# Performance work log

Measured on AMD Instinct MI355X. Metric: run time of the kernel, lower is better.

Reference implementation:

```python
import jax, jax.numpy as jnp
import numpy as np

ETA = 0.01   # Hebbian learning rate of the plasticity rule
LR = 1.0     # CircuitModel.lr


def setup_inputs() -> dict:
    key = jax.random.key(0)
    k1, k2, k3 = jax.random.split(key, 3)
    B, T, NI, NO, NOBS = 64, 256, 512, 512, 128
    X = jax.random.normal(k1, (B, T, NI), dtype=jnp.float32)
    W_init = jax.random.normal(k2, (B, NO, NI), dtype=jnp.float32) * 0.1
    observed_idx = jnp.sort(jax.random.randint(k3, (NOBS,), 0, NO))
    return {"X": X, "W_init": W_init, "observed_idx": observed_idx}


def reference(X, W_init, observed_idx):
    # X: [B,T,NI], W_init: [B,NO,NI], observed_idx: [NOBS] int
    NO = W_init.shape[1]
    mask = jnp.zeros((NO,), X.dtype).at[observed_idx].set(1.0)  # [NO]

    def step(W, x_t):
        # x_t: [B,NI]
        pre = jnp.einsum('boi,bi->bo', W, x_t)          # [B,NO]
        y = jax.nn.sigmoid(pre)
        m = y[:, observed_idx]                           # [B,NOBS] recorded before masking
        y_sparse = y * mask                              # zero unobserved outputs
        W = W * mask[None, :, None]                      # zero unobserved rows of W
        dW = ETA * (y_sparse[:, :, None] * x_t[:, None, :])  # Hebbian outer product
        return W + LR * dW, m

    _, m_traj = jax.lax.scan(step, W_init, jnp.swapaxes(X, 0, 1))  # [T,B,NOBS]
    return jnp.swapaxes(m_traj, 0, 1)  # [B,T,NOBS]
```

## Files before the change

### kernel.cpp

```cpp
#include <hip/hip_runtime.h>

#define NB   64
#define NT   256
#define NI   512
#define NO   512
#define NOBS 128
#define ETA  0.01f

typedef __attribute__((ext_vector_type(8))) short bf16x8;
typedef __attribute__((ext_vector_type(4))) float f32x4;

#define X4_COUNT  (NB*NT*NI/4)
#define WG4_COUNT (NB*NOBS*NI/4)
#define K0_TOTAL  (X4_COUNT + WG4_COUNT)

__device__ __forceinline__ unsigned short f2bf(float f) {
    unsigned int u = __float_as_uint(f);
    return (unsigned short)((u + 0x7fffu + ((u >> 16) & 1u)) >> 16);
}

__global__ __launch_bounds__(256)
void k0_convert(const float* __restrict__ X, const float* __restrict__ Wi,
                const int* __restrict__ obs,
                unsigned short* __restrict__ Xb, unsigned short* __restrict__ Wg)
{
    int idx = blockIdx.x * 256 + threadIdx.x;
    const int stride = gridDim.x * 256;
    for (; idx < K0_TOTAL; idx += stride) {
        float4 v; ushort4* dst;
        if (idx < X4_COUNT) {
            v = ((const float4*)X)[idx];
            dst = (ushort4*)Xb + idx;
        } else {
            int g = idx - X4_COUNT;
            int row = g >> 7, pos = g & 127;
            int b = row >> 7, j = row & 127;
            v = ((const float4*)(Wi + ((size_t)b * NO + obs[j]) * NI))[pos];
            dst = (ushort4*)Wg + ((size_t)row * 128 + pos);
        }
        *dst = make_ushort4(f2bf(v.x), f2bf(v.y), f2bf(v.z), f2bf(v.w));
    }
}

__global__ __launch_bounds__(256)
void k1_gemm(const unsigned short* __restrict__ Xb,
             const unsigned short* __restrict__ Wg,
             float* __restrict__ Gd, unsigned short* __restrict__ Gh,
             float* __restrict__ P0)
{
    __shared__ unsigned short As[128 * 64];
    __shared__ unsigned short Bs[128 * 64];

    const int tid  = threadIdx.x;
    const int lane = tid & 63;
    const int wv   = tid >> 6;
    const int l16  = lane & 15;
    const int quad = lane >> 4;

    const int b   = blockIdx.x & 63;
    const int sub = blockIdx.x >> 6;

    const unsigned short* xbB = Xb + (size_t)b * NT * NI;
    const unsigned short *aRows, *bRows;
    int bm = 0, bn = 0;
    if (sub < 3) {
        bm = (sub >= 1) ? 1 : 0;
        bn = (sub == 2) ? 1 : 0;
        aRows = xbB + (size_t)bm * 128 * NI;
        bRows = xbB + (size_t)bn * 128 * NI;
    } else {
        const int pb = sub - 3;
        bm = pb;
        aRows = xbB + (size_t)pb * 128 * NI;
        bRows = Wg + (size_t)b * NOBS * NI;
    }

    const int wm = (wv >> 1) * 64;
    const int wn = (wv & 1) * 64;

    f32x4 acc[4][4] = {};

    for (int kb = 0; kb < NI / 64; ++kb) {
        __syncthreads();
#pragma unroll
        for (int it = 0; it < 4; ++it) {
            const int s = it * 256 + tid;
            const int m = s >> 3, c = s & 7;
            const int slot = m * 64 + ((c ^ (m & 7)) * 8);
            const size_t goff = (size_t)m * NI + kb * 64 + c * 8;
            *(bf16x8*)&As[slot] = *(const bf16x8*)(aRows + goff);
            *(bf16x8*)&Bs[slot] = *(const bf16x8*)(bRows + goff);
        }
        __syncthreads();
#pragma unroll
        for (int ks = 0; ks < 2; ++ks) {
            const int q = ks * 4 + quad;
            bf16x8 af[4], bfr[4];
#pragma unroll
            for (int mt = 0; mt < 4; ++mt) {
                const int m = wm + mt * 16 + l16;
                af[mt] = *(const bf16x8*)&As[m * 64 + ((q ^ (m & 7)) * 8)];
            }
#pragma unroll
            for (int nt = 0; nt < 4; ++nt) {
                const int n = wn + nt * 16 + l16;
                bfr[nt] = *(const bf16x8*)&Bs[n * 64 + ((q ^ (n & 7)) * 8)];
            }
#pragma unroll
            for (int mt = 0; mt < 4; ++mt)
#pragma unroll
                for (int nt = 0; nt < 4; ++nt)
                    acc[mt][nt] = __builtin_amdgcn_mfma_f32_16x16x32_bf16(
                        af[mt], bfr[nt], acc[mt][nt], 0, 0, 0);
        }
    }

    if (sub < 3) {
        unsigned short* GhB = Gh + ((size_t)b << 16);
        float* GdB = Gd + ((size_t)b << 12);
#pragma unroll
        for (int mt = 0; mt < 4; ++mt)
#pragma unroll
            for (int nt = 0; nt < 4; ++nt) {
                const int gcol = bn * 128 + wn + nt * 16 + l16;
#pragma unroll
                for (int r = 0; r < 4; ++r) {
                    const int grow = bm * 128 + wm + mt * 16 + quad * 4 + r;
                    const float v = acc[mt][nt][r];
                    GhB[(size_t)grow * 256 + gcol] = f2bf(v);
                    if ((grow >> 4) == (gcol >> 4))
                        GdB[((grow >> 4) << 8) + ((grow & 15) << 4) + (gcol & 15)] = v;
                }
            }
    } else {
        float* Pb = P0 + (size_t)b * NT * NOBS + (size_t)bm * 128 * NOBS;
#pragma unroll
        for (int mt = 0; mt < 4; ++mt)
#pragma unroll
            for (int nt = 0; nt < 4; ++nt)
#pragma unroll
                for (int r = 0; r < 4; ++r)
                    Pb[(size_t)(wm + mt * 16 + quad * 4 + r) * NOBS
                       + wn + nt * 16 + l16] = acc[mt][nt][r];
    }
}

__global__ __launch_bounds__(512)
void k2_scan(const float* __restrict__ Gd, const unsigned short* __restrict__ Gh,
             const float* __restrict__ P0, float* __restrict__ out)
{
    __shared__ float gdiag[16 * 16 * 16];
    __shared__ float preS[16 * 32];
    __shared__ unsigned int ybf2[2 * 8 * 32];

    const int tid  = threadIdx.x;
    const int lane = tid & 63;
    const int l16  = lane & 15;
    const int quad = lane >> 4;
    const int w    = __builtin_amdgcn_readfirstlane(tid >> 6);

    const int b  = blockIdx.x & 63;
    const int jg = blockIdx.x >> 6;

    const float* Pb = P0 + (size_t)b * NT * NOBS + jg * 32;
    const unsigned short* GhB = Gh + ((size_t)b << 16);
    float* ob = out + (size_t)b * NT * NOBS + jg * 32;

    {
        const f32x4* gs = (const f32x4*)(Gd + ((size_t)b << 12));
        ((f32x4*)gdiag)[tid]       = gs[tid];
        ((f32x4*)gdiag)[512 + tid] = gs[512 + tid];
    }

    f32x4 acc[2][2];
#pragma unroll
    for (int s2 = 0; s2 < 2; ++s2)
#pragma unroll
        for (int nt = 0; nt < 2; ++nt)
#pragma unroll
            for (int r = 0; r < 4; ++r)
                acc[s2][nt][r] =
                    Pb[(size_t)(w * 32 + s2 * 16 + quad * 4 + r) * NOBS
                       + nt * 16 + l16];

#pragma unroll
    for (int c = 0; c < 16; ++c) {
        const int cp = c & 1;
        if (w == (c >> 1)) {
#pragma unroll
            for (int nt = 0; nt < 2; ++nt)
#pragma unroll
                for (int r = 0; r < 4; ++r)
                    preS[(quad * 4 + r) * 32 + nt * 16 + l16] = acc[cp][nt][r];
        }
        __syncthreads();
        if (w == (c >> 1) && lane < 32) {
            const int j = lane;
            float p[16];
#pragma unroll
            for (int u = 0; u < 16; ++u) p[u] = preS[u * 32 + j];
            const float* gdc = gdiag + c * 256;
            float eprev = 0.f;
#pragma unroll
            for (int u = 0; u < 16; ++u) {
                const float y = 1.f / (1.f + __expf(-p[u]));
                ob[(size_t)(c * 16 + u) * NOBS + j] = y;
                const float e = ETA * y;
#pragma unroll
                for (int v = u + 1; v < 16; ++v)
                    p[v] = fmaf(e, gdc[u * 16 + v], p[v]);
                if (u & 1)
                    ybf2[cp * 256 + (u >> 1) * 32 + j] =
                        (unsigned)f2bf(eprev) | ((unsigned)f2bf(e) << 16);
                else
                    eprev = e;
            }
        }
        __syncthreads();
        if (c < 15) {
            union { bf16x8 v; unsigned int d[4]; } B0, B1;
#pragma unroll
            for (int p2 = 0; p2 < 4; ++p2) { B0.d[p2] = 0; B1.d[p2] = 0; }
            if (quad < 2) {
#pragma unroll
                for (int p2 = 0; p2 < 4; ++p2) {
                    B0.d[p2] = ybf2[cp * 256 + (quad * 4 + p2) * 32 + l16];
                    B1.d[p2] = ybf2[cp * 256 + (quad * 4 + p2) * 32 + 16 + l16];
                }
            }
#pragma unroll
            for (int s2 = 0; s2 < 2; ++s2) {
                const int T = 2 * w + s2;
                if (T > c) {
                    union { bf16x8 v; unsigned int d[4]; } A;
#pragma unroll
                    for (int p2 = 0; p2 < 4; ++p2) A.d[p2] = 0;
                    if (quad < 2)
                        A.v = *(const bf16x8*)(GhB + (size_t)(T * 16 + l16) * 256
                                               + c * 16 + quad * 8);
                    acc[s2][0] = __builtin_amdgcn_mfma_f32_16x16x32_bf16(
                        A.v, B0.v, acc[s2][0], 0, 0, 0);
                    acc[s2][1] = __builtin_amdgcn_mfma_f32_16x16x32_bf16(
                        A.v, B1.v, acc[s2][1], 0, 0, 0);
                }
            }
        }
    }
}

extern "C" void kernel_launch(void* const* d_in, const int* in_sizes, int n_in,
                              void* d_out, int out_size, void* d_ws, size_t ws_size,
                              hipStream_t stream)
{
    const float* X   = (const float*)d_in[0];
    const float* Wi  = (const float*)d_in[1];
    const int*   obs = (const int*)d_in[2];
    float*       out = (float*)d_out;

    float*          Gd = (float*)d_ws;
    float*          P0 = (float*)((char*)d_ws + (1u << 20));
    unsigned short* Gh = (unsigned short*)((char*)d_ws + (9u << 20));
    unsigned short* Xb = (unsigned short*)((char*)d_ws + (17u << 20));
    unsigned short* Wg = (unsigned short*)((char*)d_ws + (33u << 20));

    hipLaunchKernelGGL(k0_convert, dim3(3072), dim3(256), 0, stream,
                       X, Wi, obs, Xb, Wg);
    hipLaunchKernelGGL(k1_gemm, dim3(NB * 5), dim3(256), 0, stream,
                       Xb, Wg, Gd, Gh, P0);
    hipLaunchKernelGGL(k2_scan, dim3(NB * 4), dim3(512), 0, stream,
                       Gd, Gh, P0, out);
}
```

Baseline: 168.1 us.

## Collapse scan kernel to one wavefront with register-held bf16 Hebbian history

Rewrites k2_scan from 8 wavefronts with two block barriers per chunk to a single 64-lane wavefront. Each 16-step chunk gathers its correction from earlier chunks by MFMA over a K=32 history kept in registers (Bf). That history is refreshed every two chunks, and the odd chunk adds a half-K MFMA for its immediate predecessor. This removes __syncthreads overhead and cross-wave handoff latency on the sequential path. In exchange the block is much smaller, the GPU has far fewer active waves, and register pressure rises.

```diff
diff --git a/kernel.cpp b/kernel.cpp
--- a/kernel.cpp
+++ b/kernel.cpp
@@ -145,19 +145,17 @@
     }
 }
 
-__global__ __launch_bounds__(512)
+__global__ __launch_bounds__(64)
 void k2_scan(const float* __restrict__ Gd, const unsigned short* __restrict__ Gh,
              const float* __restrict__ P0, float* __restrict__ out)
 {
-    __shared__ float gdiag[16 * 16 * 16];
-    __shared__ float preS[16 * 32];
-    __shared__ unsigned int ybf2[2 * 8 * 32];
-
-    const int tid  = threadIdx.x;
-    const int lane = tid & 63;
+    __shared__ float gdiag[16 * 256];
+    __shared__ unsigned short ybuf[32 * 32];
+    __shared__ float preS[16 * 33];
+
+    const int lane = threadIdx.x;
     const int l16  = lane & 15;
     const int quad = lane >> 4;
-    const int w    = __builtin_amdgcn_readfirstlane(tid >> 6);
 
     const int b  = blockIdx.x & 63;
     const int jg = blockIdx.x >> 6;
@@ -168,82 +166,90 @@
 
     {
         const f32x4* gs = (const f32x4*)(Gd + ((size_t)b << 12));
-        ((f32x4*)gdiag)[tid]       = gs[tid];
-        ((f32x4*)gdiag)[512 + tid] = gs[512 + tid];
-    }
-
-    f32x4 acc[2][2];
-#pragma unroll
-    for (int s2 = 0; s2 < 2; ++s2)
+#pragma unroll
+        for (int p = 0; p < 16; ++p)
+            ((f32x4*)gdiag)[p * 64 + lane] = gs[p * 64 + lane];
+    }
+
+    bf16x8 Bf[8][2];
+
+#pragma unroll
+    for (int T = 0; T < 16; ++T) {
+        f32x4 acc[2];
 #pragma unroll
         for (int nt = 0; nt < 2; ++nt)
 #pragma unroll
             for (int r = 0; r < 4; ++r)
-                acc[s2][nt][r] =
-                    Pb[(size_t)(w * 32 + s2 * 16 + quad * 4 + r) * NOBS
-                       + nt * 16 + l16];
-
-#pragma unroll
-    for (int c = 0; c < 16; ++c) {
-        const int cp = c & 1;
-        if (w == (c >> 1)) {
-#pragma unroll
-            for (int nt = 0; nt < 2; ++nt)
-#pragma unroll
-                for (int r = 0; r < 4; ++r)
-                    preS[(quad * 4 + r) * 32 + nt * 16 + l16] = acc[cp][nt][r];
-        }
-        __syncthreads();
-        if (w == (c >> 1) && lane < 32) {
+                acc[nt][r] = Pb[(size_t)(T * 16 + quad * 4 + r) * NOBS
+                                + nt * 16 + l16];
+
+#pragma unroll
+        for (int p = 0; p < 8; ++p)
+            if (p < (T >> 1)) {
+                const bf16x8 A = *(const bf16x8*)(
+                    GhB + (size_t)(T * 16 + l16) * 256 + p * 32 + quad * 8);
+                acc[0] = __builtin_amdgcn_mfma_f32_16x16x32_bf16(
+                    A, Bf[p][0], acc[0], 0, 0, 0);
+                acc[1] = __builtin_amdgcn_mfma_f32_16x16x32_bf16(
+                    A, Bf[p][1], acc[1], 0, 0, 0);
+            }
+
+        if (T & 1) {
+            union { bf16x8 v; unsigned int d[4]; } A, B0, B1;
+#pragma unroll
+            for (int q = 0; q < 4; ++q) { A.d[q] = 0; B0.d[q] = 0; B1.d[q] = 0; }
+            if (quad < 2) {
+                A.v = *(const bf16x8*)(
+                    GhB + (size_t)(T * 16 + l16) * 256 + (T - 1) * 16 + quad * 8);
+#pragma unroll
+                for (int jj = 0; jj < 8; ++jj) {
+                    const unsigned short y0 = ybuf[(quad * 8 + jj) * 32 + l16];
+                    const unsigned short y1 = ybuf[(quad * 8 + jj) * 32 + 16 + l16];
+                    B0.v[jj] = (short)y0;
+                    B1.v[jj] = (short)y1;
+                }
+            }
+            acc[0] = __builtin_amdgcn_mfma_f32_16x16x32_bf16(
+                A.v, B0.v, acc[0], 0, 0, 0);
+            acc[1] = __builtin_amdgcn_mfma_f32_16x16x32_bf16(
+                A.v, B1.v, acc[1], 0, 0, 0);
+        }
+
+#pragma unroll
+        for (int nt = 0; nt < 2; ++nt)
+#pragma unroll
+            for (int r = 0; r < 4; ++r)
+                preS[(quad * 4 + r) * 33 + nt * 16 + l16] = acc[nt][r];
+
+        if (lane < 32) {
             const int j = lane;
-            float p[16];
-#pragma unroll
-            for (int u = 0; u < 16; ++u) p[u] = preS[u * 32 + j];
-            const float* gdc = gdiag + c * 256;
-            float eprev = 0.f;
+            float pv[16];
+#pragma unroll
+            for (int u = 0; u < 16; ++u) pv[u] = preS[u * 33 + j];
+            const float* gd = gdiag + T * 256;
+            const int yrow = (T & 1) * 16;
 #pragma unroll
             for (int u = 0; u < 16; ++u) {
-                const float y = 1.f / (1.f + __expf(-p[u]));
-                ob[(size_t)(c * 16 + u) * NOBS + j] = y;
+                const float y = 1.f / (1.f + __expf(-pv[u]));
+                ob[(size_t)(T * 16 + u) * NOBS + j] = y;
                 const float e = ETA * y;
+                ybuf[(yrow + u) * 32 + j] = f2bf(e);
 #pragma unroll
                 for (int v = u + 1; v < 16; ++v)
-                    p[v] = fmaf(e, gdc[u * 16 + v], p[v]);
-                if (u & 1)
-                    ybf2[cp * 256 + (u >> 1) * 32 + j] =
-                        (unsigned)f2bf(eprev) | ((unsigned)f2bf(e) << 16);
-                else
-                    eprev = e;
-            }
-        }
-        __syncthreads();
-        if (c < 15) {
-            union { bf16x8 v; unsigned int d[4]; } B0, B1;
-#pragma unroll
-            for (int p2 = 0; p2 < 4; ++p2) { B0.d[p2] = 0; B1.d[p2] = 0; }
-            if (quad < 2) {
-#pragma unroll
-                for (int p2 = 0; p2 < 4; ++p2) {
-                    B0.d[p2] = ybf2[cp * 256 + (quad * 4 + p2) * 32 + l16];
-                    B1.d[p2] = ybf2[cp * 256 + (quad * 4 + p2) * 32 + 16 + l16];
-                }
-            }
-#pragma unroll
-            for (int s2 = 0; s2 < 2; ++s2) {
-                const int T = 2 * w + s2;
-                if (T > c) {
-                    union { bf16x8 v; unsigned int d[4]; } A;
-#pragma unroll
-                    for (int p2 = 0; p2 < 4; ++p2) A.d[p2] = 0;
-                    if (quad < 2)
-                        A.v = *(const bf16x8*)(GhB + (size_t)(T * 16 + l16) * 256
-                                               + c * 16 + quad * 8);
-                    acc[s2][0] = __builtin_amdgcn_mfma_f32_16x16x32_bf16(
-                        A.v, B0.v, acc[s2][0], 0, 0, 0);
-                    acc[s2][1] = __builtin_amdgcn_mfma_f32_16x16x32_bf16(
-                        A.v, B1.v, acc[s2][1], 0, 0, 0);
-                }
-            }
+                    pv[v] = fmaf(e, gd[u * 16 + v], pv[v]);
+            }
+        }
+
+        if (T & 1) {
+            const int P = T >> 1;
+            bf16x8 b0, b1;
+#pragma unroll
+            for (int jj = 0; jj < 8; ++jj) {
+                b0[jj] = (short)ybuf[(quad * 8 + jj) * 32 + l16];
+                b1[jj] = (short)ybuf[(quad * 8 + jj) * 32 + 16 + l16];
+            }
+            Bf[P][0] = b0;
+            Bf[P][1] = b1;
         }
     }
 }
@@ -267,6 +273,6 @@
                        X, Wi, obs, Xb, Wg);
     hipLaunchKernelGGL(k1_gemm, dim3(NB * 5), dim3(256), 0, stream,
                        Xb, Wg, Gd, Gh, P0);
-    hipLaunchKernelGGL(k2_scan, dim3(NB * 4), dim3(512), 0, stream,
+    hipLaunchKernelGGL(k2_scan, dim3(NB * 4), dim3(64), 0, stream,
                        Gd, Gh, P0, out);
 }
```

Measured after the change: 170.5 us. No clear change (+1.4%).
